# Performance work log

Measured on AMD Instinct MI355X. Metric: run time of the kernel, lower is better.

## Reference

```python
import math
import jax, jax.numpy as jnp
import numpy as np

NUM_BUCKETS = 32
MAX_DISTANCE = 128
N_HEADS = 16
D_KV = 64


def _relative_position_bucket(relative_position, num_buckets=NUM_BUCKETS, max_distance=MAX_DISTANCE):
    # bidirectional (encoder) version, faithful to T5Attention._relative_position_bucket
    nb = num_buckets // 2
    rel_buckets = (relative_position > 0).astype(jnp.int32) * nb
    rp = jnp.abs(relative_position)
    max_exact = nb // 2
    is_small = rp < max_exact
    # log-spaced buckets for large distances; clamp arg of log to >=1 to avoid -inf
    rp_large = max_exact + (
        jnp.log(jnp.maximum(rp, 1).astype(jnp.float32) / max_exact)
        / math.log(max_distance / max_exact)
        * (nb - max_exact)
    ).astype(jnp.int32)
    rp_large = jnp.minimum(rp_large, nb - 1)
    return rel_buckets + jnp.where(is_small, rp, rp_large)


def setup_inputs() -> dict:
    key = jax.random.key(0)
    ks = jax.random.split(key, 6)
    B, S, D = 2, 2048, 1024
    scale = 0.02
    return {
        "hidden_states": jax.random.normal(ks[0], (B, S, D), dtype=jnp.float32),
        "Wq": jax.random.normal(ks[1], (D, N_HEADS * D_KV), dtype=jnp.float32) * scale,
        "Wk": jax.random.normal(ks[2], (D, N_HEADS * D_KV), dtype=jnp.float32) * scale,
        "Wv": jax.random.normal(ks[3], (D, N_HEADS * D_KV), dtype=jnp.float32) * scale,
        "Wo": jax.random.normal(ks[4], (N_HEADS * D_KV, D), dtype=jnp.float32) * scale,
        "rel_bias": jax.random.normal(ks[5], (NUM_BUCKETS, N_HEADS), dtype=jnp.float32),
    }


def reference(hidden_states, Wq, Wk, Wv, Wo, rel_bias):
    B, S, D = hidden_states.shape
    H, dk = N_HEADS, D_KV
    q = (hidden_states @ Wq).reshape(B, S, H, dk)
    k = (hidden_states @ Wk).reshape(B, S, H, dk)
    v = (hidden_states @ Wv).reshape(B, S, H, dk)

    pos = jnp.arange(S)
    relative_position = pos[None, :] - pos[:, None]          # [S_q, S_k]
    buckets = _relative_position_bucket(relative_position)    # [S_q, S_k]
    bias = rel_bias[buckets].transpose(2, 0, 1)               # [H, S_q, S_k]

    # T5 attention: NO 1/sqrt(d) scaling
    scores = jnp.einsum('bqhd,bkhd->bhqk', q, k) + bias[None]
    attn = jax.nn.softmax(scores, axis=-1)
    ctx = jnp.einsum('bhqk,bkhd->bqhd', attn, v).reshape(B, S, H * dk)
    return ctx @ Wo
```

## Files before the change

### kernel.cpp

```cpp
#include <hip/hip_runtime.h>
#include <stdint.h>

#define S_LEN 2048
#define NH 16
#define NB_DELTA (2*S_LEN-1)
#define FST 72

typedef __attribute__((ext_vector_type(8))) __bf16 bf16x8;
typedef __attribute__((ext_vector_type(4))) float f32x4;

__device__ __forceinline__ unsigned short f2bf(float f){
    union { float f; unsigned int u; } v; v.f = f;
    unsigned int u = v.u;
    return (unsigned short)((u + 0x7FFFu + ((u >> 16) & 1u)) >> 16);
}
__device__ __forceinline__ unsigned short f2bf_fast(float f){
    union { float f; unsigned int u; } v; v.f = f;
    return (unsigned short)((v.u + 0x8000u) >> 16);
}

__device__ __forceinline__ void gload16(const void* g, void* l){
    __builtin_amdgcn_global_load_lds(
        (const __attribute__((address_space(1))) void*)(uintptr_t)g,
        (__attribute__((address_space(3))) void*)(uintptr_t)l, 16, 0, 0);
}

__global__ __launch_bounds__(256) void bias_table_kernel(const float* __restrict__ rel_bias,
                                                         float* __restrict__ biasT){
    int t = blockIdx.x * blockDim.x + threadIdx.x;
    if (t >= NB_DELTA) return;
    int delta = t - (S_LEN - 1);
    int bucket = (delta > 0) ? 16 : 0;
    int a = delta < 0 ? -delta : delta;
    int b;
    if (a < 8) b = a;
    else {
        int bl = 33 - __builtin_clz(a * a);
        b = bl < 15 ? bl : 15;
    }
    bucket += b;
    for (int h = 0; h < NH; h++)
        biasT[h * NB_DELTA + t] = rel_bias[bucket * NH + h];
}

__global__ __launch_bounds__(256) void cast_bf16_kernel(const float* __restrict__ in,
                                                        unsigned short* __restrict__ out, int n){
    int i = (blockIdx.x * blockDim.x + threadIdx.x) * 4;
    if (i >= n) return;
    float4 f = *(const float4*)(in + i);
    ushort4 o;
    o.x = f2bf(f.x); o.y = f2bf(f.y); o.z = f2bf(f.z); o.w = f2bf(f.w);
    *(ushort4*)(out + i) = o;
}

__global__ __launch_bounds__(256) void transpose_cast4_kernel(
    const float* __restrict__ W0, const float* __restrict__ W1,
    const float* __restrict__ W2, const float* __restrict__ W3,
    unsigned short* __restrict__ D0, unsigned short* __restrict__ D1,
    unsigned short* __restrict__ D2, unsigned short* __restrict__ D3){
    const float* src; unsigned short* dst;
    switch (blockIdx.z) {
        case 0: src = W0; dst = D0; break;
        case 1: src = W1; dst = D1; break;
        case 2: src = W2; dst = D2; break;
        default: src = W3; dst = D3; break;
    }
    __shared__ float tile[32][33];
    int bx = blockIdx.x, by = blockIdx.y;
    int tx = threadIdx.x & 31, ty = threadIdx.x >> 5;
    for (int i = 0; i < 4; i++)
        tile[ty + 8*i][tx] = src[(size_t)(by*32 + ty + 8*i) * 1024 + bx*32 + tx];
    __syncthreads();
    for (int i = 0; i < 4; i++)
        dst[(size_t)(bx*32 + ty + 8*i) * 1024 + by*32 + tx] = f2bf(tile[tx][ty + 8*i]);
}

template<int MODE>
__global__ __launch_bounds__(256) void gemm_bt_kernel(const unsigned short* __restrict__ A,
                                                      const unsigned short* __restrict__ BT,
                                                      float* __restrict__ C0,
                                                      unsigned short* __restrict__ C1,
                                                      unsigned short* __restrict__ C2,
                                                      int Kdim, int ldc){
    __shared__ __align__(16) unsigned short As[128 * 32];
    __shared__ __align__(16) unsigned short Bs[128 * 32];
    const int t = threadIdx.x;
    const int wave = t >> 6, lane = t & 63;
    const int quad = lane >> 4, l16 = lane & 15;
    const int wm = (wave >> 1) * 64, wn = (wave & 1) * 64;
    const size_t row0 = (size_t)blockIdx.y * 128, col0 = (size_t)blockIdx.x * 128;

    const unsigned short* ga = A  + (row0 + wave * 32 + (lane >> 2)) * (size_t)Kdim + (lane & 3) * 8;
    const unsigned short* gb = BT + (col0 + wave * 32 + (lane >> 2)) * (size_t)Kdim + (lane & 3) * 8;
    unsigned short* la0 = &As[(wave * 32) * 32];
    unsigned short* la1 = &As[(wave * 32 + 16) * 32];
    unsigned short* lb0 = &Bs[(wave * 32) * 32];
    unsigned short* lb1 = &Bs[(wave * 32 + 16) * 32];
    const size_t rstep = (size_t)16 * Kdim;

    f32x4 acc[4][4] = {};

    for (int kt = 0; kt < Kdim; kt += 32) {
        gload16(ga + kt,         la0);
        gload16(ga + rstep + kt, la1);
        gload16(gb + kt,         lb0);
        gload16(gb + rstep + kt, lb1);
        __syncthreads();
        bf16x8 a[4], b[4];
        for (int i = 0; i < 4; i++)
            a[i] = *(const bf16x8*)(&As[(wm + i*16 + l16) * 32 + quad * 8]);
        for (int j = 0; j < 4; j++)
            b[j] = *(const bf16x8*)(&Bs[(wn + j*16 + l16) * 32 + quad * 8]);
        for (int i = 0; i < 4; i++)
            for (int j = 0; j < 4; j++)
                acc[i][j] = __builtin_amdgcn_mfma_f32_16x16x32_bf16(a[i], b[j], acc[i][j], 0, 0, 0);
        __syncthreads();
    }
    for (int i = 0; i < 4; i++)
        for (int j = 0; j < 4; j++) {
            size_t r0 = row0 + wm + i*16 + quad*4;
            size_t c  = col0 + wn + j*16 + l16;
            if (MODE == 0) {
                for (int r = 0; r < 4; r++)
                    C0[(r0 + r) * ldc + c] = acc[i][j][r];
            } else {
                if (c < 2048) {
                    for (int r = 0; r < 4; r++)
                        C1[(r0 + r) * 2048 + c] = f2bf(acc[i][j][r]);
                } else {
                    int bb = (int)(r0 >> 11);
                    int s  = (int)(r0 & 2047);
                    ushort4 pk;
                    pk.x = f2bf(acc[i][j][0]); pk.y = f2bf(acc[i][j][1]);
                    pk.z = f2bf(acc[i][j][2]); pk.w = f2bf(acc[i][j][3]);
                    *(ushort4*)(C2 + ((size_t)(bb * 1024) + (c - 2048)) * 2048 + s) = pk;
                }
            }
        }
}

__global__ __launch_bounds__(256, 4) void flash4_kernel(
    const unsigned short* __restrict__ qk,
    const unsigned short* __restrict__ vt,
    const float* __restrict__ biasT,
    unsigned short* __restrict__ ctxb)
{
    const int qt = blockIdx.x, h = blockIdx.y, b = blockIdx.z;
    const int t = threadIdx.x;
    const int w = t >> 6, lane = t & 63, quad = lane >> 4, l16 = lane & 15;
    const int q0 = qt * 128;

    __shared__ __align__(16) unsigned short smem[128 * FST];
    __shared__ __align__(16) unsigned short Pb[128 * FST];
    __shared__ float bias_s[192];
    unsigned short* Qs  = smem;
    unsigned short* Ks  = smem;
    unsigned short* Vts = smem + 64 * FST;

    for (int s = 0; s < 4; s++) {
        int g = t + s * 256;
        int r = g >> 3, c = (g & 7) * 8;
        *(int4*)&Qs[r * FST + c] =
            *(const int4*)(qk + (size_t)(b * S_LEN + q0 + r) * 2048 + h * 64 + c);
    }
    __syncthreads();
    bf16x8 qb[2][2];
    for (int nt = 0; nt < 2; nt++)
        for (int ks = 0; ks < 2; ks++)
            qb[ks][nt] = *(const bf16x8*)&Qs[(w * 32 + nt * 16 + l16) * FST + ks * 32 + quad * 8];

    float rsum[2] = {0.f, 0.f};
    f32x4 ctx[4][2] = {};

    const float* biasRow = biasT + h * NB_DELTA + 2047;

    for (int kt = 0; kt < S_LEN; kt += 64) {
        __syncthreads();
        {
            int r0 = t >> 3, c0 = (t & 7) * 8;
            int g1 = t + 256;
            int r1 = g1 >> 3, c1 = (g1 & 7) * 8;
            const unsigned short* kbase = qk + (size_t)(b * S_LEN + kt) * 2048 + 1024 + h * 64;
            *(int4*)&Ks[r0 * FST + c0] = *(const int4*)(kbase + (size_t)r0 * 2048 + c0);
            *(int4*)&Ks[r1 * FST + c1] = *(const int4*)(kbase + (size_t)r1 * 2048 + c1);
            const unsigned short* vbase = vt + (size_t)(b * 1024 + h * 64) * 2048 + kt;
            *(int4*)&Vts[r0 * FST + c0] = *(const int4*)(vbase + (size_t)r0 * 2048 + c0);
            *(int4*)&Vts[r1 * FST + c1] = *(const int4*)(vbase + (size_t)r1 * 2048 + c1);
            if (t < 192) bias_s[t] = biasRow[kt - q0 - 127 + t] - 16.0f;
        }
        __syncthreads();

        f32x4 st[4][2] = {};
        for (int ks = 0; ks < 2; ks++)
            for (int nb = 0; nb < 4; nb++) {
                bf16x8 ka = *(const bf16x8*)&Ks[(nb * 16 + l16) * FST + ks * 32 + quad * 8];
                st[nb][0] = __builtin_amdgcn_mfma_f32_16x16x32_bf16(ka, qb[ks][0], st[nb][0], 0, 0, 0);
                st[nb][1] = __builtin_amdgcn_mfma_f32_16x16x32_bf16(ka, qb[ks][1], st[nb][1], 0, 0, 0);
            }
        for (int nt = 0; nt < 2; nt++) {
            const int ib = quad * 4 + 127 - w * 32 - nt * 16 - l16;
            float rs = 0.f;
            for (int nb = 0; nb < 4; nb++) {
                float e0 = __expf(st[nb][nt][0] + bias_s[ib + nb * 16 + 0]);
                float e1 = __expf(st[nb][nt][1] + bias_s[ib + nb * 16 + 1]);
                float e2 = __expf(st[nb][nt][2] + bias_s[ib + nb * 16 + 2]);
                float e3 = __expf(st[nb][nt][3] + bias_s[ib + nb * 16 + 3]);
                rs += (e0 + e1) + (e2 + e3);
                ushort4 pk;
                pk.x = f2bf_fast(e0); pk.y = f2bf_fast(e1);
                pk.z = f2bf_fast(e2); pk.w = f2bf_fast(e3);
                *(ushort4*)&Pb[(w * 32 + nt * 16 + l16) * FST + nb * 16 + quad * 4] = pk;
            }
            rsum[nt] += rs;
        }
        for (int ks = 0; ks < 2; ks++) {
            bf16x8 pb0 = *(const bf16x8*)&Pb[(w * 32 + l16) * FST + ks * 32 + quad * 8];
            bf16x8 pb1 = *(const bf16x8*)&Pb[(w * 32 + 16 + l16) * FST + ks * 32 + quad * 8];
            for (int nd = 0; nd < 4; nd++) {
                bf16x8 va = *(const bf16x8*)&Vts[(nd * 16 + l16) * FST + ks * 32 + quad * 8];
                ctx[nd][0] = __builtin_amdgcn_mfma_f32_16x16x32_bf16(va, pb0, ctx[nd][0], 0, 0, 0);
                ctx[nd][1] = __builtin_amdgcn_mfma_f32_16x16x32_bf16(va, pb1, ctx[nd][1], 0, 0, 0);
            }
        }
    }
    for (int nt = 0; nt < 2; nt++) {
        float rs = rsum[nt];
        rs += __shfl_xor(rs, 16, 64);
        rs += __shfl_xor(rs, 32, 64);
        float inv = 1.f / rs;
        size_t row = (size_t)(b * S_LEN + q0 + w * 32 + nt * 16 + l16);
        for (int nd = 0; nd < 4; nd++) {
            ushort4 pk;
            pk.x = f2bf(ctx[nd][nt][0] * inv); pk.y = f2bf(ctx[nd][nt][1] * inv);
            pk.z = f2bf(ctx[nd][nt][2] * inv); pk.w = f2bf(ctx[nd][nt][3] * inv);
            *(ushort4*)&ctxb[row * 1024 + h * 64 + nd * 16 + quad * 4] = pk;
        }
    }
}

extern "C" void kernel_launch(void* const* d_in, const int* in_sizes, int n_in,
                              void* d_out, int out_size, void* d_ws, size_t ws_size,
                              hipStream_t stream) {
    const float* hs       = (const float*)d_in[0];
    const float* Wq       = (const float*)d_in[1];
    const float* Wk       = (const float*)d_in[2];
    const float* Wv       = (const float*)d_in[3];
    const float* Wo       = (const float*)d_in[4];
    const float* rel_bias = (const float*)d_in[5];
    float* out = (float*)d_out;

    char* ws = (char*)d_ws;
    float* biasT          = (float*)ws;           ws += 262144;
    unsigned short* hsb   = (unsigned short*)ws;  ws += 8388608;
    unsigned short* WT    = (unsigned short*)ws;  ws += 6291456;
    unsigned short* WoT   = (unsigned short*)ws;  ws += 2097152;
    unsigned short* qkbuf = (unsigned short*)ws;  ws += 16777216;
    unsigned short* Vtg   = (unsigned short*)ws;  ws += 8388608;
    unsigned short* ctxb  = (unsigned short*)ws;

    bias_table_kernel<<<(NB_DELTA + 255) / 256, 256, 0, stream>>>(rel_bias, biasT);
    cast_bf16_kernel<<<4096, 256, 0, stream>>>(hs, hsb, 4194304);
    transpose_cast4_kernel<<<dim3(32, 32, 4), 256, 0, stream>>>(
        Wq, Wk, Wv, Wo, WT, WT + 1024 * 1024, WT + 2 * 1024 * 1024, WoT);

    gemm_bt_kernel<1><<<dim3(24, 32), 256, 0, stream>>>(hsb, WT, nullptr, qkbuf, Vtg, 1024, 0);
    flash4_kernel<<<dim3(S_LEN / 128, NH, 2), 256, 0, stream>>>(qkbuf, Vtg, biasT, ctxb);
    gemm_bt_kernel<0><<<dim3(8, 32), 256, 0, stream>>>(ctxb, WoT, out, nullptr, nullptr, 1024, 1024);
}
```

Measured before the change: 226.0 us.

## Split attention over two key halves with combine pass, smaller output GEMM tile

The flash attention kernel now splits the key range into two halves, which doubles the grid from 512 to 1024 blocks. Each half writes unnormalised fp32 partial context and row sums, and a new combine kernel adds them, normalises and casts to bf16. The split works without a running max because the softmax uses a fixed offset. The output GEMM uses 64-row tiles to double its block count, and the bias-table build is fused into the cast kernel to save a launch. The cost is an extra 32 MB fp32 partial write and read plus one more kernel launch, in exchange for better CU occupancy on the attention and output GEMM stages.

```diff
diff --git a/kernel.cpp b/kernel.cpp
--- a/kernel.cpp
+++ b/kernel.cpp
@@ -25,32 +25,34 @@
         (__attribute__((address_space(3))) void*)(uintptr_t)l, 16, 0, 0);
 }
 
-__global__ __launch_bounds__(256) void bias_table_kernel(const float* __restrict__ rel_bias,
-                                                         float* __restrict__ biasT){
-    int t = blockIdx.x * blockDim.x + threadIdx.x;
-    if (t >= NB_DELTA) return;
-    int delta = t - (S_LEN - 1);
-    int bucket = (delta > 0) ? 16 : 0;
-    int a = delta < 0 ? -delta : delta;
-    int b;
-    if (a < 8) b = a;
-    else {
-        int bl = 33 - __builtin_clz(a * a);
-        b = bl < 15 ? bl : 15;
-    }
-    bucket += b;
-    for (int h = 0; h < NH; h++)
-        biasT[h * NB_DELTA + t] = rel_bias[bucket * NH + h];
-}
-
-__global__ __launch_bounds__(256) void cast_bf16_kernel(const float* __restrict__ in,
-                                                        unsigned short* __restrict__ out, int n){
+__global__ __launch_bounds__(256) void cast_bias_kernel(const float* __restrict__ in,
+                                                        unsigned short* __restrict__ out, int n,
+                                                        const float* __restrict__ rel_bias,
+                                                        float* __restrict__ biasT){
     int i = (blockIdx.x * blockDim.x + threadIdx.x) * 4;
-    if (i >= n) return;
-    float4 f = *(const float4*)(in + i);
-    ushort4 o;
-    o.x = f2bf(f.x); o.y = f2bf(f.y); o.z = f2bf(f.z); o.w = f2bf(f.w);
-    *(ushort4*)(out + i) = o;
+    if (i < n) {
+        float4 f = *(const float4*)(in + i);
+        ushort4 o;
+        o.x = f2bf(f.x); o.y = f2bf(f.y); o.z = f2bf(f.z); o.w = f2bf(f.w);
+        *(ushort4*)(out + i) = o;
+    }
+    if (blockIdx.x < 16) {
+        int t = blockIdx.x * 256 + threadIdx.x;
+        if (t < NB_DELTA) {
+            int delta = t - (S_LEN - 1);
+            int bucket = (delta > 0) ? 16 : 0;
+            int a = delta < 0 ? -delta : delta;
+            int b;
+            if (a < 8) b = a;
+            else {
+                int bl = 33 - __builtin_clz(a * a);
+                b = bl < 15 ? bl : 15;
+            }
+            bucket += b;
+            for (int h = 0; h < NH; h++)
+                biasT[h * NB_DELTA + t] = rel_bias[bucket * NH + h];
+        }
+    }
 }
 
 __global__ __launch_bounds__(256) void transpose_cast4_kernel(
@@ -75,48 +77,49 @@
         dst[(size_t)(bx*32 + ty + 8*i) * 1024 + by*32 + tx] = f2bf(tile[tx][ty + 8*i]);
 }
 
-template<int MODE>
+template<int MODE, int BM>
 __global__ __launch_bounds__(256) void gemm_bt_kernel(const unsigned short* __restrict__ A,
                                                       const unsigned short* __restrict__ BT,
                                                       float* __restrict__ C0,
                                                       unsigned short* __restrict__ C1,
                                                       unsigned short* __restrict__ C2,
                                                       int Kdim, int ldc){
-    __shared__ __align__(16) unsigned short As[128 * 32];
+    constexpr int IT = BM / 32;
+    __shared__ __align__(16) unsigned short As[BM * 32];
     __shared__ __align__(16) unsigned short Bs[128 * 32];
     const int t = threadIdx.x;
     const int wave = t >> 6, lane = t & 63;
     const int quad = lane >> 4, l16 = lane & 15;
-    const int wm = (wave >> 1) * 64, wn = (wave & 1) * 64;
-    const size_t row0 = (size_t)blockIdx.y * 128, col0 = (size_t)blockIdx.x * 128;
-
-    const unsigned short* ga = A  + (row0 + wave * 32 + (lane >> 2)) * (size_t)Kdim + (lane & 3) * 8;
+    const int wm = (wave >> 1) * (BM / 2), wn = (wave & 1) * 64;
+    const size_t row0 = (size_t)blockIdx.y * BM, col0 = (size_t)blockIdx.x * 128;
+
+    const unsigned short* ga = A  + (row0 + wave * (BM/4) + (lane >> 2)) * (size_t)Kdim + (lane & 3) * 8;
     const unsigned short* gb = BT + (col0 + wave * 32 + (lane >> 2)) * (size_t)Kdim + (lane & 3) * 8;
-    unsigned short* la0 = &As[(wave * 32) * 32];
-    unsigned short* la1 = &As[(wave * 32 + 16) * 32];
+    unsigned short* la0 = &As[(wave * (BM/4)) * 32];
+    unsigned short* la1 = &As[(wave * (BM/4) + 16) * 32];
     unsigned short* lb0 = &Bs[(wave * 32) * 32];
     unsigned short* lb1 = &Bs[(wave * 32 + 16) * 32];
     const size_t rstep = (size_t)16 * Kdim;
 
-    f32x4 acc[4][4] = {};
+    f32x4 acc[IT][4] = {};
 
     for (int kt = 0; kt < Kdim; kt += 32) {
-        gload16(ga + kt,         la0);
-        gload16(ga + rstep + kt, la1);
+        gload16(ga + kt, la0);
+        if (BM == 128) gload16(ga + rstep + kt, la1);
         gload16(gb + kt,         lb0);
         gload16(gb + rstep + kt, lb1);
         __syncthreads();
-        bf16x8 a[4], b[4];
-        for (int i = 0; i < 4; i++)
+        bf16x8 a[IT], b[4];
+        for (int i = 0; i < IT; i++)
             a[i] = *(const bf16x8*)(&As[(wm + i*16 + l16) * 32 + quad * 8]);
         for (int j = 0; j < 4; j++)
             b[j] = *(const bf16x8*)(&Bs[(wn + j*16 + l16) * 32 + quad * 8]);
-        for (int i = 0; i < 4; i++)
+        for (int i = 0; i < IT; i++)
             for (int j = 0; j < 4; j++)
                 acc[i][j] = __builtin_amdgcn_mfma_f32_16x16x32_bf16(a[i], b[j], acc[i][j], 0, 0, 0);
         __syncthreads();
     }
-    for (int i = 0; i < 4; i++)
+    for (int i = 0; i < IT; i++)
         for (int j = 0; j < 4; j++) {
             size_t r0 = row0 + wm + i*16 + quad*4;
             size_t c  = col0 + wn + j*16 + l16;
@@ -139,13 +142,16 @@
         }
 }
 
-__global__ __launch_bounds__(256, 4) void flash4_kernel(
+__global__ __launch_bounds__(256, 4) void flash5_kernel(
     const unsigned short* __restrict__ qk,
     const unsigned short* __restrict__ vt,
     const float* __restrict__ biasT,
-    unsigned short* __restrict__ ctxb)
+    float* __restrict__ ctxp,
+    float* __restrict__ rsbuf)
 {
-    const int qt = blockIdx.x, h = blockIdx.y, b = blockIdx.z;
+    const int qt = blockIdx.x, h = blockIdx.y;
+    const int b = blockIdx.z >> 1, ck = blockIdx.z & 1;
+    const int kt0 = ck << 10;
     const int t = threadIdx.x;
     const int w = t >> 6, lane = t & 63, quad = lane >> 4, l16 = lane & 15;
     const int q0 = qt * 128;
@@ -174,7 +180,7 @@
 
     const float* biasRow = biasT + h * NB_DELTA + 2047;
 
-    for (int kt = 0; kt < S_LEN; kt += 64) {
+    for (int kt = kt0; kt < kt0 + 1024; kt += 64) {
         __syncthreads();
         {
             int r0 = t >> 3, c0 = (t & 7) * 8;
@@ -223,19 +229,37 @@
             }
         }
     }
+    float* cp = ctxp + (size_t)ck * 4096 * 1024;
     for (int nt = 0; nt < 2; nt++) {
         float rs = rsum[nt];
         rs += __shfl_xor(rs, 16, 64);
         rs += __shfl_xor(rs, 32, 64);
-        float inv = 1.f / rs;
-        size_t row = (size_t)(b * S_LEN + q0 + w * 32 + nt * 16 + l16);
+        int row = b * S_LEN + q0 + w * 32 + nt * 16 + l16;
+        if (quad == 0) rsbuf[((size_t)ck * 4096 + row) * 16 + h] = rs;
         for (int nd = 0; nd < 4; nd++) {
-            ushort4 pk;
-            pk.x = f2bf(ctx[nd][nt][0] * inv); pk.y = f2bf(ctx[nd][nt][1] * inv);
-            pk.z = f2bf(ctx[nd][nt][2] * inv); pk.w = f2bf(ctx[nd][nt][3] * inv);
-            *(ushort4*)&ctxb[row * 1024 + h * 64 + nd * 16 + quad * 4] = pk;
-        }
-    }
+            float4 pv;
+            pv.x = ctx[nd][nt][0]; pv.y = ctx[nd][nt][1];
+            pv.z = ctx[nd][nt][2]; pv.w = ctx[nd][nt][3];
+            *(float4*)&cp[(size_t)row * 1024 + h * 64 + nd * 16 + quad * 4] = pv;
+        }
+    }
+}
+
+__global__ __launch_bounds__(256) void combine_kernel(const float* __restrict__ ctxp,
+                                                      const float* __restrict__ rsbuf,
+                                                      unsigned short* __restrict__ ctxb){
+    int e = blockIdx.x * 256 + threadIdx.x;
+    int row = e >> 8;
+    int c4 = (e & 255) * 4;
+    int h = c4 >> 6;
+    float l = rsbuf[(size_t)row * 16 + h] + rsbuf[((size_t)4096 + row) * 16 + h];
+    float4 a = *(const float4*)&ctxp[(size_t)row * 1024 + c4];
+    float4 bb = *(const float4*)&ctxp[(size_t)4096 * 1024 + (size_t)row * 1024 + c4];
+    float inv = 1.f / l;
+    ushort4 o;
+    o.x = f2bf((a.x + bb.x) * inv); o.y = f2bf((a.y + bb.y) * inv);
+    o.z = f2bf((a.z + bb.z) * inv); o.w = f2bf((a.w + bb.w) * inv);
+    *(ushort4*)&ctxb[(size_t)row * 1024 + c4] = o;
 }
 
 extern "C" void kernel_launch(void* const* d_in, const int* in_sizes, int n_in,
@@ -256,14 +280,16 @@
     unsigned short* WoT   = (unsigned short*)ws;  ws += 2097152;
     unsigned short* qkbuf = (unsigned short*)ws;  ws += 16777216;
     unsigned short* Vtg   = (unsigned short*)ws;  ws += 8388608;
-    unsigned short* ctxb  = (unsigned short*)ws;
-
-    bias_table_kernel<<<(NB_DELTA + 255) / 256, 256, 0, stream>>>(rel_bias, biasT);
-    cast_bf16_kernel<<<4096, 256, 0, stream>>>(hs, hsb, 4194304);
+    unsigned short* ctxb  = (unsigned short*)ws;  ws += 8388608;
+    float* ctxp           = (float*)ws;           ws += 33554432;
+    float* rsbuf          = (float*)ws;
+
+    cast_bias_kernel<<<4096, 256, 0, stream>>>(hs, hsb, 4194304, rel_bias, biasT);
     transpose_cast4_kernel<<<dim3(32, 32, 4), 256, 0, stream>>>(
         Wq, Wk, Wv, Wo, WT, WT + 1024 * 1024, WT + 2 * 1024 * 1024, WoT);
 
-    gemm_bt_kernel<1><<<dim3(24, 32), 256, 0, stream>>>(hsb, WT, nullptr, qkbuf, Vtg, 1024, 0);
-    flash4_kernel<<<dim3(S_LEN / 128, NH, 2), 256, 0, stream>>>(qkbuf, Vtg, biasT, ctxb);
-    gemm_bt_kernel<0><<<dim3(8, 32), 256, 0, stream>>>(ctxb, WoT, out, nullptr, nullptr, 1024, 1024);
-}
+    gemm_bt_kernel<1, 128><<<dim3(24, 32), 256, 0, stream>>>(hsb, WT, nullptr, qkbuf, Vtg, 1024, 0);
+    flash5_kernel<<<dim3(S_LEN / 128, NH, 4), 256, 0, stream>>>(qkbuf, Vtg, biasT, ctxp, rsbuf);
+    combine_kernel<<<4096, 256, 0, stream>>>(ctxp, rsbuf, ctxb);
+    gemm_bt_kernel<0, 64><<<dim3(8, 64), 256, 0, stream>>>(ctxb, WoT, out, nullptr, nullptr, 1024, 1024);
+}
```

Measured after the change: 211.6 us. -6.3%, faster.
